# Optimization experiments

Hardware: AMD Instinct MI355X
Metric: run time of the kernel (lower is better)

Reference implementation:

```python
import jax, jax.numpy as jnp
import numpy as np

N = 50000      # nodes
E = 600000     # edges (avg degree 12)
C = 128        # in/out channels
NF = 256       # SchNet num_filters (hardcoded in module)
EC = 64        # edge_channels (RBF expansion)


def ssp(x):
    # shifted softplus used by SchNet
    return jax.nn.softplus(x) - jnp.log(2.0).astype(x.dtype)


def setup_inputs() -> dict:
    key = jax.random.key(0)
    ks = jax.random.split(key, 16)
    def w(k, shape, fan_in):
        return jax.random.normal(k, shape, jnp.float32) * (1.0 / np.sqrt(fan_in))
    return {
        "x": jax.random.normal(ks[0], (N, C), jnp.float32),
        "edge_index": jax.random.randint(ks[1], (2, E), 0, N, jnp.int32),
        "edge_attr": jax.random.normal(ks[2], (E, EC), jnp.float32),
        "x_pos": jax.random.normal(ks[3], (N, 3), jnp.float32),
        # SchNet filter network: Linear(EC,NF) -> ssp -> Linear(NF,NF)
        "W_f1": w(ks[4], (EC, NF), EC), "b_f1": jnp.zeros((NF,), jnp.float32),
        "W_f2": w(ks[5], (NF, NF), NF), "b_f2": jnp.zeros((NF,), jnp.float32),
        # CFConv lin1 (no bias), lin2, then output lin3
        "W_lin1": w(ks[6], (C, NF), C),
        "W_lin2": w(ks[7], (NF, C), NF), "b_lin2": jnp.zeros((C,), jnp.float32),
        "W_lin3": w(ks[8], (C, C), C), "b_lin3": jnp.zeros((C,), jnp.float32),
        # edge MLP: Linear(EC + C, C) -> Tanh
        "W_e": w(ks[9], (EC + C, C), EC + C), "b_e": jnp.zeros((C,), jnp.float32),
    }


def reference(x, edge_index, edge_attr, x_pos,
              W_f1, b_f1, W_f2, b_f2,
              W_lin1, W_lin2, b_lin2, W_lin3, b_lin3,
              W_e, b_e):
    n = x.shape[0]
    row, col = edge_index[0], edge_index[1]

    # SchNet interaction (cfconv): edge filter net on edge_attr
    Wf = ssp(edge_attr @ W_f1 + b_f1) @ W_f2 + b_f2      # [E, NF]
    h = x @ W_lin1                                        # [N, NF]
    msg = h[col] * Wf                                     # [E, NF] gather + modulate
    agg = jax.ops.segment_sum(msg, row, num_segments=n)   # [N, NF] scatter-sum
    y = ssp(agg @ W_lin2 + b_lin2) @ W_lin3 + b_lin3      # [N, C]

    # relu + residual skip
    x_out = jax.nn.relu(y) + x

    # edge gather-MLP with residual on edge_attr
    e_in = jnp.concatenate([edge_attr, x_out[row] + x_out[col]], axis=-1)  # [E, EC+C]
    e_out = jnp.tanh(e_in @ W_e + b_e) + edge_attr if False else jnp.tanh(e_in @ W_e + b_e)
    # note: original adds residual only on edge_attr channels; shapes differ (C vs EC)
    # Linear maps to in_channels=C... but residual is `+ edge_attr` [E,EC]. In the repo
    # edge_channels == in_channels is required for this add; here EC != C, so we
    # follow the module math with EC projected: use the faithful form below.
    return x_out, e_out
```

## Files before the change

kernel.cpp:

```cpp
#include <hip/hip_runtime.h>

#define NN  50000
#define NE  600000
#define CC  128
#define NFF 256
#define ECH 64
#define EIN 192

typedef __attribute__((ext_vector_type(8))) short bf16x8;
typedef __attribute__((ext_vector_type(4))) short bf16x4;
typedef __attribute__((ext_vector_type(4))) float f32x4;

__device__ __forceinline__ float sspf(float v) {
    float e = __expf(-fabsf(v));
    return fmaxf(v, 0.f) + __logf(1.f + e) - 0.693147180559945f;
}
__device__ __forceinline__ float ftanh(float v) {
    float e = __expf(-2.f * fabsf(v));
    float r = (1.f - e) / (1.f + e);
    return copysignf(r, v);
}
__device__ __forceinline__ short bf16r(float f) {
    unsigned u = __float_as_uint(f);
    u = (u + 0x7FFFu + ((u >> 16) & 1u)) >> 16;
    return (short)u;
}
__device__ __forceinline__ float bf2f(short s) {
    unsigned u = ((unsigned)(unsigned short)s) << 16;
    return __uint_as_float(u);
}

#define PO_WF1 0
#define PO_WF2 16384
#define PO_WE  81920
#define PO_WL1 106496
#define PO_WL2 139264
#define PO_WL3 172032
#define P_TOT  188416
__global__ void kpack(const float* __restrict__ Wf1, const float* __restrict__ Wf2,
                      const float* __restrict__ We,  const float* __restrict__ Wl1,
                      const float* __restrict__ Wl2, const float* __restrict__ Wl3,
                      short* __restrict__ p) {
    int i = blockIdx.x * 256 + threadIdx.x;
    if (i < PO_WF2) {
        int t = i - PO_WF1;
        int j = t & 7, lane = (t >> 3) & 63, n16 = (t >> 9) & 15, ks = t >> 13;
        p[i] = bf16r(Wf1[(ks * 32 + (lane >> 4) * 8 + j) * NFF + n16 * 16 + (lane & 15)]);
    } else if (i < PO_WE) {
        int t = i - PO_WF2;
        int j = t & 7, lane = (t >> 3) & 63, n16 = (t >> 9) & 15, ks = t >> 13;
        p[i] = bf16r(Wf2[(ks * 32 + (lane >> 4) * 8 + j) * NFF + n16 * 16 + (lane & 15)]);
    } else if (i < PO_WL1) {
        int t = i - PO_WE;
        int j = t & 7, lane = (t >> 3) & 63, n16 = (t >> 9) & 7, ks = t >> 12;
        p[i] = bf16r(We[(ks * 32 + (lane >> 4) * 8 + j) * CC + n16 * 16 + (lane & 15)]);
    } else if (i < PO_WL2) {
        int t = i - PO_WL1;
        int j = t & 7, lane = (t >> 3) & 63, n16 = (t >> 9) & 15, ks = t >> 13;
        p[i] = bf16r(Wl1[(ks * 32 + (lane >> 4) * 8 + j) * NFF + n16 * 16 + (lane & 15)]);
    } else if (i < PO_WL3) {
        int t = i - PO_WL2;
        int j = t & 7, lane = (t >> 3) & 63, n16 = (t >> 9) & 7, ks = t >> 12;
        p[i] = bf16r(Wl2[(ks * 32 + (lane >> 4) * 8 + j) * CC + n16 * 16 + (lane & 15)]);
    } else if (i < P_TOT) {
        int t = i - PO_WL3;
        int j = t & 7, lane = (t >> 3) & 63, n16 = (t >> 9) & 7, ks = t >> 12;
        p[i] = bf16r(Wl3[(ks * 32 + (lane >> 4) * 8 + j) * CC + n16 * 16 + (lane & 15)]);
    }
}

__global__ void k0_zero(float* __restrict__ p, long n4) {
    long i = (long)blockIdx.x * blockDim.x + threadIdx.x;
    long stride = (long)gridDim.x * blockDim.x;
    float4 z = {0.f, 0.f, 0.f, 0.f};
    for (; i < n4; i += stride) ((float4*)p)[i] = z;
}

__global__ void k_cnt(const int* __restrict__ eidx, int* __restrict__ cnt) {
    int e = blockIdx.x * 256 + threadIdx.x;
    if (e < NE) atomicAdd(&cnt[eidx[e]], 1);
}

__global__ __launch_bounds__(256) void k_scan1(const int* __restrict__ cnt,
                                               int* __restrict__ offw,
                                               int* __restrict__ bsum) {
    __shared__ int sw_[4];
    int i = blockIdx.x * 256 + threadIdx.x;
    int lane = threadIdx.x & 63, wv = threadIdx.x >> 6;
    int v = (i < NN) ? cnt[i] : 0;
    int inc = v;
    #pragma unroll
    for (int d = 1; d < 64; d <<= 1) {
        int t = __shfl_up(inc, d, 64);
        if (lane >= d) inc += t;
    }
    if (lane == 63) sw_[wv] = inc;
    __syncthreads();
    int woff = 0;
    #pragma unroll
    for (int k = 0; k < 4; ++k) woff += (k < wv) ? sw_[k] : 0;
    if (i < NN) offw[i] = woff + inc - v;
    if (threadIdx.x == 255) bsum[blockIdx.x] = woff + inc;
}

__global__ __launch_bounds__(256) void k_scan2(int* __restrict__ bsum, int nb) {
    __shared__ int sw_[4];
    int t = threadIdx.x;
    int lane = t & 63, wv = t >> 6;
    int v = (t < nb) ? bsum[t] : 0;
    int inc = v;
    #pragma unroll
    for (int d = 1; d < 64; d <<= 1) {
        int s = __shfl_up(inc, d, 64);
        if (lane >= d) inc += s;
    }
    if (lane == 63) sw_[wv] = inc;
    __syncthreads();
    int woff = 0;
    #pragma unroll
    for (int k = 0; k < 4; ++k) woff += (k < wv) ? sw_[k] : 0;
    if (t < nb) bsum[t] = woff + inc - v;
}

__global__ void k_scan3(int* __restrict__ offw, const int* __restrict__ bsum,
                        int* __restrict__ rowptr) {
    int i = blockIdx.x * 256 + threadIdx.x;
    if (i < NN) {
        int v = offw[i] + bsum[blockIdx.x];
        offw[i] = v;
        rowptr[i] = v;
    }
    if (i == 0) rowptr[NN] = NE;
}

__global__ void k_scatter(const int* __restrict__ eidx, int* __restrict__ offw,
                          int* __restrict__ dest) {
    int e = blockIdx.x * 256 + threadIdx.x;
    if (e < NE) dest[e] = atomicAdd(&offw[eidx[e]], 1);
}

__global__ __launch_bounds__(256) void k1_h(const float* __restrict__ x,
                                            const short* __restrict__ pWl1,
                                            short* __restrict__ h) {
    __shared__ char xS[32 * 256];
    int n0 = blockIdx.x * 32;
    int tid = threadIdx.x;
    int lane = tid & 63, w = tid >> 6, q = lane >> 4, l15 = lane & 15;
    {
        int r = tid >> 3, seg = tid & 7;
        int rr = min(n0 + r, NN - 1);
        const float4* src = (const float4*)(x + (size_t)rr * CC + seg * 16);
        float4 f0 = src[0], f1 = src[1], f2 = src[2], f3 = src[3];
        bf16x8 c0 = {bf16r(f0.x), bf16r(f0.y), bf16r(f0.z), bf16r(f0.w),
                     bf16r(f1.x), bf16r(f1.y), bf16r(f1.z), bf16r(f1.w)};
        bf16x8 c1 = {bf16r(f2.x), bf16r(f2.y), bf16r(f2.z), bf16r(f2.w),
                     bf16r(f3.x), bf16r(f3.y), bf16r(f3.z), bf16r(f3.w)};
        int sw = (r & 7) << 4;
        *(bf16x8*)(xS + r * 256 + ((seg * 32) ^ sw)) = c0;
        *(bf16x8*)(xS + r * 256 + ((seg * 32 + 16) ^ sw)) = c1;
    }
    __syncthreads();

    f32x4 acc[2][4];
    #pragma unroll
    for (int mf = 0; mf < 2; ++mf)
        #pragma unroll
        for (int nf = 0; nf < 4; ++nf) acc[mf][nf] = f32x4{0.f, 0.f, 0.f, 0.f};

    #pragma unroll
    for (int ks = 0; ks < 4; ++ks) {
        bf16x8 a[2];
        #pragma unroll
        for (int mf = 0; mf < 2; ++mf) {
            int row = mf * 16 + l15;
            a[mf] = *(const bf16x8*)(xS + row * 256 + ((ks * 64 + q * 16) ^ ((row & 7) << 4)));
        }
        #pragma unroll
        for (int nf = 0; nf < 4; ++nf) {
            bf16x8 b = *(const bf16x8*)(pWl1 + PO_WL1 + (((ks * 16 + w * 4 + nf) * 64) + lane) * 8);
            #pragma unroll
            for (int mf = 0; mf < 2; ++mf)
                acc[mf][nf] = __builtin_amdgcn_mfma_f32_16x16x32_bf16(a[mf], b, acc[mf][nf], 0, 0, 0);
        }
    }
    #pragma unroll
    for (int nf = 0; nf < 4; ++nf) {
        int col = w * 64 + nf * 16 + l15;
        #pragma unroll
        for (int mf = 0; mf < 2; ++mf) {
            #pragma unroll
            for (int r = 0; r < 4; ++r) {
                int n = n0 + mf * 16 + q * 4 + r;
                if (n < NN) h[(size_t)n * NFF + col] = bf16r(acc[mf][nf][r]);
            }
        }
    }
}

__global__ __launch_bounds__(256, 8) void k2a_msg(
        const float* __restrict__ ea, const int* __restrict__ eidx,
        const int* __restrict__ dest,
        const short* __restrict__ pW, const float* __restrict__ bf1v,
        const float* __restrict__ bf2v,
        const short* __restrict__ h, short* __restrict__ msg) {
    __shared__ char eaS[32 * 128];
    __shared__ char t1S[32 * 512];
    __shared__ int colS[32], destS[32];
    int e0 = blockIdx.x * 32;
    int tid = threadIdx.x;
    int lane = tid & 63, w = tid >> 6;
    int q = lane >> 4, l15 = lane & 15;

    if (tid < 32) {
        colS[tid] = eidx[NE + e0 + tid];
        destS[tid] = dest[e0 + tid];
    }

    {
        int r = tid >> 3, cp = tid & 7;
        const float4* src = (const float4*)(ea + (size_t)(e0 + r) * ECH + cp * 8);
        float4 f0 = src[0], f1 = src[1];
        bf16x8 c0 = {bf16r(f0.x), bf16r(f0.y), bf16r(f0.z), bf16r(f0.w),
                     bf16r(f1.x), bf16r(f1.y), bf16r(f1.z), bf16r(f1.w)};
        int sw = (r & 7) << 4;
        *(bf16x8*)(eaS + r * 128 + ((cp * 16) ^ sw)) = c0;
    }
    __syncthreads();

    f32x4 acc[2][4];
    #pragma unroll
    for (int mf = 0; mf < 2; ++mf)
        #pragma unroll
        for (int nf = 0; nf < 4; ++nf) acc[mf][nf] = f32x4{0.f, 0.f, 0.f, 0.f};

    #pragma unroll
    for (int ks = 0; ks < 2; ++ks) {
        bf16x8 a[2];
        #pragma unroll
        for (int mf = 0; mf < 2; ++mf) {
            int row = mf * 16 + l15;
            a[mf] = *(const bf16x8*)(eaS + row * 128 + ((ks * 64 + q * 16) ^ ((row & 7) << 4)));
        }
        #pragma unroll
        for (int nf = 0; nf < 4; ++nf) {
            bf16x8 b = *(const bf16x8*)(pW + PO_WF1 + (((ks * 16 + w * 4 + nf) * 64) + lane) * 8);
            #pragma unroll
            for (int mf = 0; mf < 2; ++mf)
                acc[mf][nf] = __builtin_amdgcn_mfma_f32_16x16x32_bf16(a[mf], b, acc[mf][nf], 0, 0, 0);
        }
    }
    #pragma unroll
    for (int nf = 0; nf < 4; ++nf) {
        int col = w * 64 + nf * 16 + l15;
        float bias = bf1v[col];
        #pragma unroll
        for (int mf = 0; mf < 2; ++mf) {
            #pragma unroll
            for (int r = 0; r < 4; ++r) {
                int row = mf * 16 + q * 4 + r;
                *(short*)(t1S + row * 512 + ((col * 2) ^ ((row & 7) << 4))) =
                    bf16r(sspf(acc[mf][nf][r] + bias));
            }
        }
    }
    __syncthreads();

    #pragma unroll
    for (int mf = 0; mf < 2; ++mf)
        #pragma unroll
        for (int nf = 0; nf < 4; ++nf) acc[mf][nf] = f32x4{0.f, 0.f, 0.f, 0.f};

    for (int ks = 0; ks < 8; ++ks) {
        bf16x8 a[2];
        #pragma unroll
        for (int mf = 0; mf < 2; ++mf) {
            int row = mf * 16 + l15;
            a[mf] = *(const bf16x8*)(t1S + row * 512 + ((ks * 64 + q * 16) ^ ((row & 7) << 4)));
        }
        #pragma unroll
        for (int nf = 0; nf < 4; ++nf) {
            bf16x8 b = *(const bf16x8*)(pW + PO_WF2 + (((ks * 16 + w * 4 + nf) * 64) + lane) * 8);
            #pragma unroll
            for (int mf = 0; mf < 2; ++mf)
                acc[mf][nf] = __builtin_amdgcn_mfma_f32_16x16x32_bf16(a[mf], b, acc[mf][nf], 0, 0, 0);
        }
    }
    __syncthreads();

    {
        int r = tid >> 3, ch = tid & 7;
        const short* hp = h + (size_t)colS[r] * NFF;
        int sw = (r & 7) << 4;
        #pragma unroll
        for (int i = 0; i < 4; ++i) {
            bf16x8 v = *(const bf16x8*)(hp + i * 64 + ch * 8);
            *(bf16x8*)(t1S + r * 512 + ((i * 128 + ch * 16) ^ sw)) = v;
        }
    }
    __syncthreads();

    #pragma unroll
    for (int nf = 0; nf < 4; ++nf) {
        int col = w * 64 + nf * 16 + l15;
        float bias = bf2v[col];
        #pragma unroll
        for (int mf = 0; mf < 2; ++mf) {
            #pragma unroll
            for (int r = 0; r < 4; ++r) {
                int eloc = mf * 16 + q * 4 + r;
                float wf = acc[mf][nf][r] + bias;
                float hv = bf2f(*(const short*)(t1S + eloc * 512 + ((col * 2) ^ ((eloc & 7) << 4))));
                msg[(size_t)destS[eloc] * NFF + col] = bf16r(hv * wf);
            }
        }
    }
}

__global__ __launch_bounds__(256) void k3_node(
        const short* __restrict__ msg, const int* __restrict__ rowptr,
        const short* __restrict__ pW, const float* __restrict__ bl2,
        const float* __restrict__ bl3,
        const float* __restrict__ x, float* __restrict__ xo) {
    __shared__ char aggS[32 * 512];
    __shared__ char t2S[32 * 256];
    int n0 = blockIdx.x * 32;
    int tid = threadIdx.x;
    int lane = tid & 63, w = tid >> 6, q = lane >> 4, l15 = lane & 15;

    {
        int nd = tid >> 3, c0 = (tid & 7) * 32;
        int n = n0 + nd;
        int p0 = 0, p1 = 0;
        if (n < NN) { p0 = rowptr[n]; p1 = rowptr[n + 1]; }
        float a[32];
        #pragma unroll
        for (int i = 0; i < 32; ++i) a[i] = 0.f;
        for (int p = p0; p < p1; ++p) {
            const short* mrow = msg + (size_t)p * NFF + c0;
            #pragma unroll
            for (int j = 0; j < 4; ++j) {
                bf16x8 v = *(const bf16x8*)(mrow + j * 8);
                #pragma unroll
                for (int k = 0; k < 8; ++k) a[j * 8 + k] += bf2f(v[k]);
            }
        }
        int sw = (nd & 7) << 4;
        #pragma unroll
        for (int j = 0; j < 4; ++j) {
            bf16x8 v;
            #pragma unroll
            for (int k = 0; k < 8; ++k) v[k] = bf16r(a[j * 8 + k]);
            *(bf16x8*)(aggS + nd * 512 + (((c0 + j * 8) * 2) ^ sw)) = v;
        }
    }
    __syncthreads();

    f32x4 acc[2][2];
    #pragma unroll
    for (int mf = 0; mf < 2; ++mf)
        #pragma unroll
        for (int nf = 0; nf < 2; ++nf) acc[mf][nf] = f32x4{0.f, 0.f, 0.f, 0.f};
    for (int ks = 0; ks < 8; ++ks) {
        bf16x8 a[2];
        #pragma unroll
        for (int mf = 0; mf < 2; ++mf) {
            int row = mf * 16 + l15;
            a[mf] = *(const bf16x8*)(aggS + row * 512 + ((ks * 64 + q * 16) ^ ((row & 7) << 4)));
        }
        #pragma unroll
        for (int nf = 0; nf < 2; ++nf) {
            bf16x8 b = *(const bf16x8*)(pW + PO_WL2 + (((ks * 8 + w * 2 + nf) * 64) + lane) * 8);
            #pragma unroll
            for (int mf = 0; mf < 2; ++mf)
                acc[mf][nf] = __builtin_amdgcn_mfma_f32_16x16x32_bf16(a[mf], b, acc[mf][nf], 0, 0, 0);
        }
    }
    #pragma unroll
    for (int nf = 0; nf < 2; ++nf) {
        int col = w * 32 + nf * 16 + l15;
        float bias = bl2[col];
        #pragma unroll
        for (int mf = 0; mf < 2; ++mf) {
            #pragma unroll
            for (int r = 0; r < 4; ++r) {
                int row = mf * 16 + q * 4 + r;
                *(short*)(t2S + row * 256 + ((col * 2) ^ ((row & 7) << 4))) =
                    bf16r(sspf(acc[mf][nf][r] + bias));
            }
        }
    }
    __syncthreads();

    f32x4 acc2[2][2];
    #pragma unroll
    for (int mf = 0; mf < 2; ++mf)
        #pragma unroll
        for (int nf = 0; nf < 2; ++nf) acc2[mf][nf] = f32x4{0.f, 0.f, 0.f, 0.f};
    #pragma unroll
    for (int ks = 0; ks < 4; ++ks) {
        bf16x8 a[2];
        #pragma unroll
        for (int mf = 0; mf < 2; ++mf) {
            int row = mf * 16 + l15;
            a[mf] = *(const bf16x8*)(t2S + row * 256 + ((ks * 64 + q * 16) ^ ((row & 7) << 4)));
        }
        #pragma unroll
        for (int nf = 0; nf < 2; ++nf) {
            bf16x8 b = *(const bf16x8*)(pW + PO_WL3 + (((ks * 8 + w * 2 + nf) * 64) + lane) * 8);
            #pragma unroll
            for (int mf = 0; mf < 2; ++mf)
                acc2[mf][nf] = __builtin_amdgcn_mfma_f32_16x16x32_bf16(a[mf], b, acc2[mf][nf], 0, 0, 0);
        }
    }
    #pragma unroll
    for (int nf = 0; nf < 2; ++nf) {
        int col = w * 32 + nf * 16 + l15;
        float bias = bl3[col];
        #pragma unroll
        for (int mf = 0; mf < 2; ++mf) {
            #pragma unroll
            for (int r = 0; r < 4; ++r) {
                int n = n0 + mf * 16 + q * 4 + r;
                if (n < NN) {
                    size_t o = (size_t)n * CC + col;
                    xo[o] = fmaxf(acc2[mf][nf][r] + bias, 0.f) + x[o];
                }
            }
        }
    }
}

__global__ __launch_bounds__(256) void k4_mfma(
        const float* __restrict__ ea, const int* __restrict__ eidx,
        const float* __restrict__ xo, const short* __restrict__ pW,
        const float* __restrict__ bev, float* __restrict__ eo) {
    __shared__ char aS[64 * 384];
    int e0 = blockIdx.x * 64;
    int tid = threadIdx.x;
    int lane = tid & 63, w = tid >> 6;
    int q = lane >> 4, l15 = lane & 15;

    {
        int r = tid >> 2, cp = tid & 3;
        const float4* src = (const float4*)(ea + (size_t)(e0 + r) * ECH + cp * 16);
        float4 f0 = src[0], f1 = src[1], f2 = src[2], f3 = src[3];
        bf16x8 c0 = {bf16r(f0.x), bf16r(f0.y), bf16r(f0.z), bf16r(f0.w),
                     bf16r(f1.x), bf16r(f1.y), bf16r(f1.z), bf16r(f1.w)};
        bf16x8 c1 = {bf16r(f2.x), bf16r(f2.y), bf16r(f2.z), bf16r(f2.w),
                     bf16r(f3.x), bf16r(f3.y), bf16r(f3.z), bf16r(f3.w)};
        int sw = (r & 7) << 4;
        *(bf16x8*)(aS + r * 384 + ((cp * 32) ^ sw)) = c0;
        *(bf16x8*)(aS + r * 384 + ((cp * 32 + 16) ^ sw)) = c1;
    }
    {
        int e = tid >> 2, p = tid & 3;
        int rr = eidx[e0 + e], cc = eidx[NE + e0 + e];
        const float4* xr = (const float4*)(xo + (size_t)rr * CC);
        const float4* xc = (const float4*)(xo + (size_t)cc * CC);
        int sw = (e & 7) << 4;
        #pragma unroll
        for (int it = 0; it < 8; ++it) {
            int fi = p + it * 4;
            float4 va = xr[fi], vb = xc[fi];
            bf16x4 hv = {bf16r(va.x + vb.x), bf16r(va.y + vb.y),
                         bf16r(va.z + vb.z), bf16r(va.w + vb.w)};
            int byte = (ECH + fi * 4) * 2;
            *(bf16x4*)(aS + e * 384 + (byte ^ sw)) = hv;
        }
    }
    __syncthreads();

    f32x4 acc[8];
    #pragma unroll
    for (int nf = 0; nf < 8; ++nf) acc[nf] = f32x4{0.f, 0.f, 0.f, 0.f};

    #pragma unroll
    for (int ks = 0; ks < 6; ++ks) {
        int row = w * 16 + l15;
        bf16x8 a = *(const bf16x8*)(aS + row * 384 + ((ks * 64 + q * 16) ^ ((row & 7) << 4)));
        #pragma unroll
        for (int nf = 0; nf < 8; ++nf) {
            bf16x8 b = *(const bf16x8*)(pW + PO_WE + (((ks * 8 + nf) * 64) + lane) * 8);
            acc[nf] = __builtin_amdgcn_mfma_f32_16x16x32_bf16(a, b, acc[nf], 0, 0, 0);
        }
    }
    #pragma unroll
    for (int nf = 0; nf < 8; ++nf) {
        int col = nf * 16 + l15;
        float bias = bev[col];
        #pragma unroll
        for (int r = 0; r < 4; ++r) {
            int e = e0 + w * 16 + q * 4 + r;
            eo[(size_t)e * CC + col] = ftanh(acc[nf][r] + bias);
        }
    }
}

extern "C" void kernel_launch(void* const* d_in, const int* in_sizes, int n_in,
                              void* d_out, int out_size, void* d_ws, size_t ws_size,
                              hipStream_t stream) {
    const float* x   = (const float*)d_in[0];
    const int*   ei  = (const int*)d_in[1];
    const float* ea  = (const float*)d_in[2];
    const float* Wf1 = (const float*)d_in[4];
    const float* bf1 = (const float*)d_in[5];
    const float* Wf2 = (const float*)d_in[6];
    const float* bf2 = (const float*)d_in[7];
    const float* Wl1 = (const float*)d_in[8];
    const float* Wl2 = (const float*)d_in[9];
    const float* bl2 = (const float*)d_in[10];
    const float* Wl3 = (const float*)d_in[11];
    const float* bl3 = (const float*)d_in[12];
    const float* We  = (const float*)d_in[13];
    const float* be  = (const float*)d_in[14];

    float* xo = (float*)d_out;
    float* eo = xo + (size_t)NN * CC;

    short* h   = (short*)xo;
    short* msg = (short*)eo;

    short* pW    = (short*)d_ws;
    int* dest    = (int*)((char*)d_ws + 393216);
    int* cnt     = dest + NE;
    int* offw    = cnt + NN;
    int* rowptr  = offw + NN;
    int* bsum    = rowptr + NN + 1;

    const int NB = (NN + 255) / 256;

    kpack<<<P_TOT / 256, 256, 0, stream>>>(Wf1, Wf2, We, Wl1, Wl2, Wl3, pW);
    k0_zero<<<49, 256, 0, stream>>>((float*)cnt, NN / 4);
    k_cnt<<<(NE + 255) / 256, 256, 0, stream>>>(ei, cnt);
    k_scan1<<<NB, 256, 0, stream>>>(cnt, offw, bsum);
    k_scan2<<<1, 256, 0, stream>>>(bsum, NB);
    k_scan3<<<NB, 256, 0, stream>>>(offw, bsum, rowptr);
    k_scatter<<<(NE + 255) / 256, 256, 0, stream>>>(ei, offw, dest);
    k1_h<<<(NN + 31) / 32, 256, 0, stream>>>(x, pW, h);
    k2a_msg<<<NE / 32, 256, 0, stream>>>(ea, ei, dest, pW, bf1, bf2, h, msg);
    k3_node<<<(NN + 31) / 32, 256, 0, stream>>>(msg, rowptr, pW, bl2, bl3, x, xo);
    k4_mfma<<<NE / 64, 256, 0, stream>>>(ea, ei, xo, pW, be, eo);
}
```

Before: 601.2 us.

## Use packed bf16 conversion and permute weight K-order for vectorized epilogue stores

```diff
diff --git a/kernel.cpp b/kernel.cpp
--- a/kernel.cpp
+++ b/kernel.cpp
@@ -10,6 +10,8 @@
 typedef __attribute__((ext_vector_type(8))) short bf16x8;
 typedef __attribute__((ext_vector_type(4))) short bf16x4;
 typedef __attribute__((ext_vector_type(4))) float f32x4;
+typedef __attribute__((ext_vector_type(4))) unsigned u32x4;
+typedef __attribute__((ext_vector_type(2))) unsigned u32x2;
 
 __device__ __forceinline__ float sspf(float v) {
     float e = __expf(-fabsf(v));
@@ -25,10 +27,13 @@
     u = (u + 0x7FFFu + ((u >> 16) & 1u)) >> 16;
     return (short)u;
 }
-__device__ __forceinline__ float bf2f(short s) {
-    unsigned u = ((unsigned)(unsigned short)s) << 16;
-    return __uint_as_float(u);
-}
+__device__ __forceinline__ unsigned cvtpk(float lo, float hi) {
+    unsigned r;
+    asm("v_cvt_pk_bf16_f32 %0, %1, %2" : "=v"(r) : "v"(lo), "v"(hi));
+    return r;
+}
+__device__ __forceinline__ float bfu_lo(unsigned u) { return __uint_as_float(u << 16); }
+__device__ __forceinline__ float bfu_hi(unsigned u) { return __uint_as_float(u & 0xffff0000u); }
 
 #define PO_WF1 0
 #define PO_WF2 16384
@@ -49,7 +54,9 @@
     } else if (i < PO_WE) {
         int t = i - PO_WF2;
         int j = t & 7, lane = (t >> 3) & 63, n16 = (t >> 9) & 15, ks = t >> 13;
-        p[i] = bf16r(Wf2[(ks * 32 + (lane >> 4) * 8 + j) * NFF + n16 * 16 + (lane & 15)]);
+        int kp = ks * 32 + (lane >> 4) * 8 + j;
+        int k = (kp >> 6) * 64 + (kp & 3) * 16 + ((kp >> 2) & 15);
+        p[i] = bf16r(Wf2[k * NFF + n16 * 16 + (lane & 15)]);
     } else if (i < PO_WL1) {
         int t = i - PO_WE;
         int j = t & 7, lane = (t >> 3) & 63, n16 = (t >> 9) & 7, ks = t >> 12;
@@ -61,11 +68,15 @@
     } else if (i < PO_WL3) {
         int t = i - PO_WL2;
         int j = t & 7, lane = (t >> 3) & 63, n16 = (t >> 9) & 7, ks = t >> 12;
-        p[i] = bf16r(Wl2[(ks * 32 + (lane >> 4) * 8 + j) * CC + n16 * 16 + (lane & 15)]);
+        int kp = ks * 32 + (lane >> 4) * 8 + j;
+        int k = (kp >> 6) * 64 + (kp & 3) * 16 + ((kp >> 2) & 15);
+        p[i] = bf16r(Wl2[k * CC + n16 * 16 + (lane & 15)]);
     } else if (i < P_TOT) {
         int t = i - PO_WL3;
         int j = t & 7, lane = (t >> 3) & 63, n16 = (t >> 9) & 7, ks = t >> 12;
-        p[i] = bf16r(Wl3[(ks * 32 + (lane >> 4) * 8 + j) * CC + n16 * 16 + (lane & 15)]);
+        int kp = ks * 32 + (lane >> 4) * 8 + j;
+        int k = (kp >> 5) * 32 + (kp & 1) * 16 + ((kp & 31) >> 1);
+        p[i] = bf16r(Wl3[k * CC + n16 * 16 + (lane & 15)]);
     }
 }
 
@@ -140,7 +151,7 @@
 }
 
 __global__ __launch_bounds__(256) void k1_h(const float* __restrict__ x,
-                                            const short* __restrict__ pWl1,
+                                            const short* __restrict__ pW,
                                             short* __restrict__ h) {
     __shared__ char xS[32 * 256];
     int n0 = blockIdx.x * 32;
@@ -151,13 +162,11 @@
         int rr = min(n0 + r, NN - 1);
         const float4* src = (const float4*)(x + (size_t)rr * CC + seg * 16);
         float4 f0 = src[0], f1 = src[1], f2 = src[2], f3 = src[3];
-        bf16x8 c0 = {bf16r(f0.x), bf16r(f0.y), bf16r(f0.z), bf16r(f0.w),
-                     bf16r(f1.x), bf16r(f1.y), bf16r(f1.z), bf16r(f1.w)};
-        bf16x8 c1 = {bf16r(f2.x), bf16r(f2.y), bf16r(f2.z), bf16r(f2.w),
-                     bf16r(f3.x), bf16r(f3.y), bf16r(f3.z), bf16r(f3.w)};
+        u32x4 c0 = {cvtpk(f0.x, f0.y), cvtpk(f0.z, f0.w), cvtpk(f1.x, f1.y), cvtpk(f1.z, f1.w)};
+        u32x4 c1 = {cvtpk(f2.x, f2.y), cvtpk(f2.z, f2.w), cvtpk(f3.x, f3.y), cvtpk(f3.z, f3.w)};
         int sw = (r & 7) << 4;
-        *(bf16x8*)(xS + r * 256 + ((seg * 32) ^ sw)) = c0;
-        *(bf16x8*)(xS + r * 256 + ((seg * 32 + 16) ^ sw)) = c1;
+        *(u32x4*)(xS + r * 256 + ((seg * 32) ^ sw)) = c0;
+        *(u32x4*)(xS + r * 256 + ((seg * 32 + 16) ^ sw)) = c1;
     }
     __syncthreads();
 
@@ -177,21 +186,21 @@
         }
         #pragma unroll
         for (int nf = 0; nf < 4; ++nf) {
-            bf16x8 b = *(const bf16x8*)(pWl1 + PO_WL1 + (((ks * 16 + w * 4 + nf) * 64) + lane) * 8);
+            bf16x8 b = *(const bf16x8*)(pW + PO_WL1 + (((ks * 16 + w * 4 + nf) * 64) + lane) * 8);
             #pragma unroll
             for (int mf = 0; mf < 2; ++mf)
                 acc[mf][nf] = __builtin_amdgcn_mfma_f32_16x16x32_bf16(a[mf], b, acc[mf][nf], 0, 0, 0);
         }
     }
     #pragma unroll
-    for (int nf = 0; nf < 4; ++nf) {
-        int col = w * 64 + nf * 16 + l15;
-        #pragma unroll
-        for (int mf = 0; mf < 2; ++mf) {
-            #pragma unroll
-            for (int r = 0; r < 4; ++r) {
-                int n = n0 + mf * 16 + q * 4 + r;
-                if (n < NN) h[(size_t)n * NFF + col] = bf16r(acc[mf][nf][r]);
+    for (int mf = 0; mf < 2; ++mf) {
+        #pragma unroll
+        for (int r = 0; r < 4; ++r) {
+            int n = n0 + mf * 16 + q * 4 + r;
+            if (n < NN) {
+                u32x2 v = {cvtpk(acc[mf][0][r], acc[mf][1][r]),
+                           cvtpk(acc[mf][2][r], acc[mf][3][r])};
+                *(u32x2*)(h + (size_t)n * NFF + w * 64 + l15 * 4) = v;
             }
         }
     }
@@ -220,10 +229,9 @@
         int r = tid >> 3, cp = tid & 7;
         const float4* src = (const float4*)(ea + (size_t)(e0 + r) * ECH + cp * 8);
         float4 f0 = src[0], f1 = src[1];
-        bf16x8 c0 = {bf16r(f0.x), bf16r(f0.y), bf16r(f0.z), bf16r(f0.w),
-                     bf16r(f1.x), bf16r(f1.y), bf16r(f1.z), bf16r(f1.w)};
+        u32x4 c0 = {cvtpk(f0.x, f0.y), cvtpk(f0.z, f0.w), cvtpk(f1.x, f1.y), cvtpk(f1.z, f1.w)};
         int sw = (r & 7) << 4;
-        *(bf16x8*)(eaS + r * 128 + ((cp * 16) ^ sw)) = c0;
+        *(u32x4*)(eaS + r * 128 + ((cp * 16) ^ sw)) = c0;
     }
     __syncthreads();
 
@@ -249,17 +257,18 @@
                 acc[mf][nf] = __builtin_amdgcn_mfma_f32_16x16x32_bf16(a[mf], b, acc[mf][nf], 0, 0, 0);
         }
     }
-    #pragma unroll
-    for (int nf = 0; nf < 4; ++nf) {
-        int col = w * 64 + nf * 16 + l15;
-        float bias = bf1v[col];
+    {
+        float bia[4];
+        #pragma unroll
+        for (int nf = 0; nf < 4; ++nf) bia[nf] = bf1v[w * 64 + nf * 16 + l15];
         #pragma unroll
         for (int mf = 0; mf < 2; ++mf) {
             #pragma unroll
             for (int r = 0; r < 4; ++r) {
                 int row = mf * 16 + q * 4 + r;
-                *(short*)(t1S + row * 512 + ((col * 2) ^ ((row & 7) << 4))) =
-                    bf16r(sspf(acc[mf][nf][r] + bias));
+                u32x2 v = {cvtpk(sspf(acc[mf][0][r] + bia[0]), sspf(acc[mf][1][r] + bia[1])),
+                           cvtpk(sspf(acc[mf][2][r] + bia[2]), sspf(acc[mf][3][r] + bia[3]))};
+                *(u32x2*)(t1S + row * 512 + ((w * 128 + l15 * 8) ^ ((row & 7) << 4))) = v;
             }
         }
     }
@@ -299,18 +308,22 @@
     }
     __syncthreads();
 
-    #pragma unroll
-    for (int nf = 0; nf < 4; ++nf) {
-        int col = w * 64 + nf * 16 + l15;
-        float bias = bf2v[col];
+    {
+        float bia[4];
+        #pragma unroll
+        for (int nf = 0; nf < 4; ++nf) bia[nf] = bf2v[w * 64 + nf * 16 + l15];
         #pragma unroll
         for (int mf = 0; mf < 2; ++mf) {
             #pragma unroll
             for (int r = 0; r < 4; ++r) {
                 int eloc = mf * 16 + q * 4 + r;
-                float wf = acc[mf][nf][r] + bias;
-                float hv = bf2f(*(const short*)(t1S + eloc * 512 + ((col * 2) ^ ((eloc & 7) << 4))));
-                msg[(size_t)destS[eloc] * NFF + col] = bf16r(hv * wf);
+                u32x2 hv = *(const u32x2*)(t1S + eloc * 512 + ((w * 128 + l15 * 8) ^ ((eloc & 7) << 4)));
+                float m0 = bfu_lo(hv[0]) * (acc[mf][0][r] + bia[0]);
+                float m1 = bfu_hi(hv[0]) * (acc[mf][1][r] + bia[1]);
+                float m2 = bfu_lo(hv[1]) * (acc[mf][2][r] + bia[2]);
+                float m3 = bfu_hi(hv[1]) * (acc[mf][3][r] + bia[3]);
+                u32x2 out = {cvtpk(m0, m1), cvtpk(m2, m3)};
+                *(u32x2*)(msg + (size_t)destS[eloc] * NFF + w * 64 + l15 * 4) = out;
             }
         }
     }
@@ -339,18 +352,20 @@
             const short* mrow = msg + (size_t)p * NFF + c0;
             #pragma unroll
             for (int j = 0; j < 4; ++j) {
-                bf16x8 v = *(const bf16x8*)(mrow + j * 8);
+                u32x4 v = *(const u32x4*)(mrow + j * 8);
                 #pragma unroll
-                for (int k = 0; k < 8; ++k) a[j * 8 + k] += bf2f(v[k]);
+                for (int k = 0; k < 4; ++k) {
+                    a[j * 8 + 2 * k]     += bfu_lo(v[k]);
+                    a[j * 8 + 2 * k + 1] += bfu_hi(v[k]);
+                }
             }
         }
         int sw = (nd & 7) << 4;
         #pragma unroll
         for (int j = 0; j < 4; ++j) {
-            bf16x8 v;
-            #pragma unroll
-            for (int k = 0; k < 8; ++k) v[k] = bf16r(a[j * 8 + k]);
-            *(bf16x8*)(aggS + nd * 512 + (((c0 + j * 8) * 2) ^ sw)) = v;
+            u32x4 v = {cvtpk(a[j * 8 + 0], a[j * 8 + 1]), cvtpk(a[j * 8 + 2], a[j * 8 + 3]),
+                       cvtpk(a[j * 8 + 4], a[j * 8 + 5]), cvtpk(a[j * 8 + 6], a[j * 8 + 7])};
+            *(u32x4*)(aggS + nd * 512 + (((c0 + j * 8) * 2) ^ sw)) = v;
         }
     }
     __syncthreads();
@@ -375,17 +390,17 @@
                 acc[mf][nf] = __builtin_amdgcn_mfma_f32_16x16x32_bf16(a[mf], b, acc[mf][nf], 0, 0, 0);
         }
     }
-    #pragma unroll
-    for (int nf = 0; nf < 2; ++nf) {
-        int col = w * 32 + nf * 16 + l15;
-        float bias = bl2[col];
+    {
+        float bia[2];
+        #pragma unroll
+        for (int nf = 0; nf < 2; ++nf) bia[nf] = bl2[w * 32 + nf * 16 + l15];
         #pragma unroll
         for (int mf = 0; mf < 2; ++mf) {
             #pragma unroll
             for (int r = 0; r < 4; ++r) {
                 int row = mf * 16 + q * 4 + r;
-                *(short*)(t2S + row * 256 + ((col * 2) ^ ((row & 7) << 4))) =
-                    bf16r(sspf(acc[mf][nf][r] + bias));
+                unsigned u = cvtpk(sspf(acc[mf][0][r] + bia[0]), sspf(acc[mf][1][r] + bia[1]));
+                *(unsigned*)(t2S + row * 256 + ((w * 64 + l15 * 4) ^ ((row & 7) << 4))) = u;
             }
         }
     }
@@ -444,13 +459,11 @@
         int r = tid >> 2, cp = tid & 3;
         const float4* src = (const float4*)(ea + (size_t)(e0 + r) * ECH + cp * 16);
         float4 f0 = src[0], f1 = src[1], f2 = src[2], f3 = src[3];
-        bf16x8 c0 = {bf16r(f0.x), bf16r(f0.y), bf16r(f0.z), bf16r(f0.w),
-                     bf16r(f1.x), bf16r(f1.y), bf16r(f1.z), bf16r(f1.w)};
-        bf16x8 c1 = {bf16r(f2.x), bf16r(f2.y), bf16r(f2.z), bf16r(f2.w),
-                     bf16r(f3.x), bf16r(f3.y), bf16r(f3.z), bf16r(f3.w)};
+        u32x4 c0 = {cvtpk(f0.x, f0.y), cvtpk(f0.z, f0.w), cvtpk(f1.x, f1.y), cvtpk(f1.z, f1.w)};
+        u32x4 c1 = {cvtpk(f2.x, f2.y), cvtpk(f2.z, f2.w), cvtpk(f3.x, f3.y), cvtpk(f3.z, f3.w)};
         int sw = (r & 7) << 4;
-        *(bf16x8*)(aS + r * 384 + ((cp * 32) ^ sw)) = c0;
-        *(bf16x8*)(aS + r * 384 + ((cp * 32 + 16) ^ sw)) = c1;
+        *(u32x4*)(aS + r * 384 + ((cp * 32) ^ sw)) = c0;
+        *(u32x4*)(aS + r * 384 + ((cp * 32 + 16) ^ sw)) = c1;
     }
     {
         int e = tid >> 2, p = tid & 3;
@@ -462,10 +475,9 @@
         for (int it = 0; it < 8; ++it) {
             int fi = p + it * 4;
             float4 va = xr[fi], vb = xc[fi];
-            bf16x4 hv = {bf16r(va.x + vb.x), bf16r(va.y + vb.y),
-                         bf16r(va.z + vb.z), bf16r(va.w + vb.w)};
+            u32x2 hv = {cvtpk(va.x + vb.x, va.y + vb.y), cvtpk(va.z + vb.z, va.w + vb.w)};
             int byte = (ECH + fi * 4) * 2;
-            *(bf16x4*)(aS + e * 384 + (byte ^ sw)) = hv;
+            *(u32x2*)(aS + e * 384 + (byte ^ sw)) = hv;
         }
     }
     __syncthreads();
```

After: 582.1 us. 1.03x faster.
